# Optimization experiments

Hardware: AMD Instinct MI355X
Metric: run time of the kernel (lower is better)

## Reference

```python
import jax, jax.numpy as jnp
import numpy as np

B, N, F, K, H = 2, 1024, 64, 8, 4
M1 = K + 1                # 9
M2 = (F - 1) * K + 1      # 505
TEMP = 1.0


def setup_inputs() -> dict:
    key = jax.random.key(0)
    ks = jax.random.split(key, 8)
    x = jax.random.normal(ks[0], (B, N, F), dtype=jnp.float32)
    # Bernoulli(0.05) dense adjacency
    adj = (jax.random.uniform(ks[1], (B, N, N)) < 0.05).astype(jnp.float32)
    mask = jnp.ones((B, N), dtype=jnp.float32)
    Wl = jax.random.normal(ks[2], (F, K * H), dtype=jnp.float32) * 0.05
    bl = jnp.zeros((K * H,), dtype=jnp.float32)
    Wr = jax.random.normal(ks[3], (F, K * H), dtype=jnp.float32) * 0.05
    br = jnp.zeros((K * H,), dtype=jnp.float32)
    # fixed affine layer: y = x @ aff_w + aff_b, aff_w[:, :F] = -I, aff_b[M2] = 1
    aff_w = jnp.zeros((F, M1 * M2), dtype=jnp.float32).at[:, :F].set(-jnp.eye(F, dtype=jnp.float32))
    aff_b = jnp.zeros((M1 * M2,), dtype=jnp.float32).at[M2].set(1.0)
    Wm = jax.random.normal(ks[4], (M1 * M2, F), dtype=jnp.float32) * 0.02
    bm = jnp.zeros((F,), dtype=jnp.float32)
    return dict(x=x, adj=adj, mask=mask, Wl=Wl, bl=bl, Wr=Wr, br=br,
                aff_w=aff_w, aff_b=aff_b, Wm=Wm, bm=bm)


def reference(x, adj, mask, Wl, bl, Wr, br, aff_w, aff_b, Wm, bm):
    # --- multi-head edge attention ---
    x_l = (x @ Wl + bl).reshape(B, N, K, H)   # [B,N,K,H]
    x_r = (x @ Wr + br).reshape(B, N, K, H)
    # scores[b,i,j,n,g] = leaky_relu(x_l[b,j] + x_r[b,i]) / temp
    scores = jax.nn.leaky_relu(x_l[:, None, :, :, :] + x_r[:, :, None, :, :]) / TEMP  # [B,N,N,K,H]
    attn_mask = mask[:, None, :] * mask[:, :, None]                # [B,N,N]
    scores = jnp.where(attn_mask[..., None, None] == 0, -1e9, scores)
    att = jax.nn.softmax(scores, axis=2)                           # softmax over source nodes j
    att = jnp.maximum(att * adj[..., None, None], 1e-6)            # clamp(min=1e-6) STE trick
    att = att / jnp.sum(att, axis=2, keepdims=True)                # renormalize
    # --- attention-weighted neighbor gather ---
    x_h = x.reshape(B, N, H, F // H)
    agg = jnp.einsum('bjgk,bijng->bingk', x_h, att).reshape(B, N, K, F)  # [B,N,K,F]
    # --- fixed affine + FFT log-domain geometric mean ---
    x_aff = (agg @ aff_w + aff_b).reshape(B, N, K, M1, M2)
    x_fft = jnp.fft.fft2(x_aff)                                    # over (M1,M2)
    mag = jnp.exp(jnp.mean(jnp.log(jnp.abs(x_fft) + 1e-6), axis=2))  # [B,N,M1,M2]
    ang = jnp.sum(jnp.angle(x_fft), axis=2)
    x_agg = jnp.fft.ifft2(mag * jnp.exp(1j * ang)).real.reshape(B, N, M1 * M2)
    # --- output MLP + node mask ---
    out = x_agg @ Wm + bm
    return out * mask[..., None]
```

## Files before the change

kernel.cpp:

```cpp
#include <hip/hip_runtime.h>
#include <math.h>

#define NN 1024
#define FD 64
#define CH 32
#define M1D 9
#define M2D 505
#define QH 253
#define THALF 2273
#define KPAD 4608
#define KSPLIT 16
#define KCHUNK 288
#define G1SZ 291456
#define G1KS 8

#define FSQRT(x) __builtin_amdgcn_sqrtf(x)
#define FRCP(x)  __builtin_amdgcn_rcpf(x)

typedef short short8 __attribute__((ext_vector_type(8)));
typedef float f32x4 __attribute__((ext_vector_type(4)));

__device__ __forceinline__ unsigned short f2bf(float x) {
    unsigned int u = __builtin_bit_cast(unsigned int, x);
    return (unsigned short)((u + 0x7FFFu + ((u >> 16) & 1u)) >> 16);
}

#define OFF_WP    1024
#define OFF_SUMX  1056
#define OFF_G1    1184
#define OFF_GMT   292640
#define OFF_XL    440096
#define OFF_XR    505632
#define OFF_AGG   571168
#define OFF_PART  1619744
#define OFF_Y     3716896
#define OFF_A2    8435488
#define OFF_WT    16824096
#define OFF_G1P   16856864

__global__ __launch_bounds__(256) void build_tw_kernel(float* __restrict__ T,
                                                       float* __restrict__ Wt,
                                                       float* __restrict__ wp,
                                                       float* __restrict__ sumx) {
    int idx = blockIdx.x * 256 + threadIdx.x;
    if (blockIdx.x == 0) {
        if (threadIdx.x < M1D) {
            float ang = (float)threadIdx.x * (-6.2831853f / 9.0f);
            float s, c; __sincosf(ang, &s, &c);
            wp[2*threadIdx.x] = c; wp[2*threadIdx.x+1] = s;
        }
        if (threadIdx.x >= 64 && threadIdx.x < 192) sumx[threadIdx.x - 64] = 0.f;
    }
    if (idx < 506 * 512) {
        int r = idx >> 9, m2 = idx & 511;
        float v = 0.f;
        if (m2 < M2D) {
            int q = r >> 1;
            int t = (q * m2) % M2D;
            float ang = (float)t * (-6.2831853f / 505.0f);
            float s, c; __sincosf(ang, &s, &c);
            v = (r & 1) ? -s : c;
        }
        T[idx] = v;
    } else if (idx < 506 * 512 + 64 * 512) {
        int i2 = idx - 506 * 512;
        int m = i2 >> 9, col = i2 & 511;
        float v = 0.f;
        if (col < 506) {
            int q = col >> 1;
            int t = (q * m) % M2D;
            float ang = (float)t * (-6.2831853f / 505.0f);
            float s, c; __sincosf(ang, &s, &c);
            v = (col & 1) ? s : c;
        }
        Wt[i2] = v;
    }
}

__global__ __launch_bounds__(64) void proj_kernel(const float* __restrict__ x,
                                                  const float* __restrict__ Wl, const float* __restrict__ bl,
                                                  const float* __restrict__ Wr, const float* __restrict__ br,
                                                  float* __restrict__ xl, float* __restrict__ xr,
                                                  float* __restrict__ sumx) {
    int blk = blockIdx.x, tid = threadIdx.x;
    if (blk >= 2048) {
        int bb = blk - 2048;
        int b = bb >> 4, chunk = bb & 15;
        const float* xb = x + (size_t)b * NN * FD;
        float acc = 0.f;
        int j0 = chunk * 64;
        #pragma unroll 4
        for (int j = j0; j < j0 + 64; j++) acc += xb[j*FD + tid];
        atomicAdd(&sumx[b*FD + tid], acc);
        return;
    }
    int node = blk;
    __shared__ float xrow[FD];
    xrow[tid] = x[(size_t)node*FD + tid];
    __syncthreads();
    int c = tid & 31;
    const float* W = (tid < 32) ? Wl : Wr;
    float acc = (tid < 32) ? bl[c] : br[c];
    #pragma unroll
    for (int f = 0; f < FD; f++) acc += xrow[f] * W[f*CH + c];
    float* dst = (tid < 32) ? xl : xr;
    dst[(size_t)node*CH + c] = acc;
}

__global__ __launch_bounds__(256) void g1_gemm_kernel(const float* __restrict__ T,
                                                      const float* __restrict__ Wm,
                                                      float* __restrict__ G1p) {
    int mt = blockIdx.x, m1 = blockIdx.y, ks = blockIdx.z;
    int tid = threadIdx.x;
    __shared__ float As[64][68];
    __shared__ float Bs[64][64];
    int r0 = mt * 64, k0 = ks * 64;
    const float* Wmb = Wm + (size_t)m1 * M2D * FD;
    float ra[16], rb[16];
    #pragma unroll
    for (int i = 0; i < 16; i++) {
        int l = tid + i*256;
        int r = l >> 6, k = l & 63;
        int rr = r0 + r;
        ra[i] = (rr < 506) ? T[(size_t)rr*512 + k0 + k] : 0.f;
    }
    #pragma unroll
    for (int i = 0; i < 16; i++) {
        int l = tid + i*256;
        int k = l >> 6, f = l & 63;
        int krow = k0 + k;
        rb[i] = (krow < M2D) ? Wmb[(size_t)krow*FD + f] : 0.f;
    }
    #pragma unroll
    for (int i = 0; i < 16; i++) {
        int l = tid + i*256;
        As[l & 63][l >> 6] = ra[i];
    }
    #pragma unroll
    for (int i = 0; i < 16; i++) {
        int l = tid + i*256;
        Bs[l >> 6][l & 63] = rb[i];
    }
    __syncthreads();
    float acc[4][4] = {{0.f}};
    int tm = (tid >> 4) * 4, tf = (tid & 15) * 4;
    #pragma unroll 8
    for (int k = 0; k < 64; k++) {
        float4 a = *(const float4*)&As[k][tm];
        float4 b = *(const float4*)&Bs[k][tf];
        acc[0][0] += a.x*b.x; acc[0][1] += a.x*b.y; acc[0][2] += a.x*b.z; acc[0][3] += a.x*b.w;
        acc[1][0] += a.y*b.x; acc[1][1] += a.y*b.y; acc[1][2] += a.y*b.z; acc[1][3] += a.y*b.w;
        acc[2][0] += a.z*b.x; acc[2][1] += a.z*b.y; acc[2][2] += a.z*b.z; acc[2][3] += a.z*b.w;
        acc[3][0] += a.w*b.x; acc[3][1] += a.w*b.y; acc[3][2] += a.w*b.z; acc[3][3] += a.w*b.w;
    }
    float* G1k = G1p + (size_t)ks * G1SZ;
    #pragma unroll
    for (int i = 0; i < 4; i++) {
        int r = r0 + tm + i;
        if (r >= 506) continue;
        int q = r >> 1, reim = r & 1;
        size_t base = (size_t)(m1*QH + q) * 128;
        #pragma unroll
        for (int j = 0; j < 4; j++)
            G1k[base + (tf + j)*2 + reim] = acc[i][j];
    }
}

__global__ __launch_bounds__(256) void g1_reduce_kernel(const float* __restrict__ G1p,
                                                        float* __restrict__ G1) {
    int idx = blockIdx.x * 256 + threadIdx.x;
    if (idx >= G1SZ/4) return;
    const float4* p = (const float4*)G1p;
    float4 s = p[idx];
    #pragma unroll
    for (int ks = 1; ks < G1KS; ks++) {
        float4 v = p[(size_t)ks*(G1SZ/4) + idx];
        s.x += v.x; s.y += v.y; s.z += v.z; s.w += v.w;
    }
    ((float4*)G1)[idx] = s;
}

__global__ __launch_bounds__(64) void gmat_kernel(const float* __restrict__ G1,
                                                  const float* __restrict__ wp,
                                                  unsigned short* __restrict__ GmT) {
    int t = blockIdx.x;
    int f = threadIdx.x;
    if (t >= THALF) {
        *(unsigned int*)&GmT[(size_t)f*KPAD + 2*t] = 0u;
        return;
    }
    int p, q;
    if (t < QH) { p = 0; q = t; }
    else { int u = t - QH; p = 1 + u / M2D; q = u % M2D; }
    float gr = 0.f, gi = 0.f;
    #pragma unroll
    for (int m1 = 0; m1 < M1D; m1++) {
        float ar, ai;
        if (q < QH) { size_t o = ((size_t)(m1*QH + q)*FD + f)*2; ar = G1[o]; ai = G1[o+1]; }
        else        { size_t o = ((size_t)(m1*QH + (M2D - q))*FD + f)*2; ar = G1[o]; ai = -G1[o+1]; }
        int pm = (p * m1) % M1D;
        float cr = wp[2*pm], ci = -wp[2*pm+1];
        gr += ar*cr - ai*ci;
        gi += ar*ci + ai*cr;
    }
    float scale = (t == 0) ? (1.0f/4545.0f) : (2.0f/4545.0f);
    unsigned int pk = (unsigned int)f2bf(gr*scale) | ((unsigned int)f2bf(-gi*scale) << 16);
    *(unsigned int*)&GmT[(size_t)f*KPAD + 2*t] = pk;
}

__global__ __launch_bounds__(256) void attn_agg_kernel(const float* __restrict__ x,
                                                       const float* __restrict__ adj,
                                                       const float* __restrict__ xl,
                                                       const float* __restrict__ xr,
                                                       const float* __restrict__ sumx,
                                                       float* __restrict__ agg) {
    int node = blockIdx.x;
    int b = node >> 10;
    int tid = threadIdx.x;
    __shared__ float xr_s[CH], Zinv[CH], Sinv[CH];
    __shared__ float red16[16][CH];
    __shared__ int act_list[NN + 8];
    __shared__ int act_n;
    __shared__ float qv2[64][CH];

    if (tid < CH) xr_s[tid] = xr[(size_t)node*CH + tid];
    if (tid == 0) act_n = 0;
    __syncthreads();

    int c = tid & 31, jl = tid >> 5;
    const float* xlb = xl + ((size_t)b << 10) * CH;
    const float* adjrow = adj + (size_t)node * NN;

    int c2 = tid & 15, jl16 = tid >> 4;
    const float2* xlb2 = (const float2*)xlb;
    float xrcx = xr_s[2*c2], xrcy = xr_s[2*c2+1];
    float zx = 0.f, zy = 0.f;
    for (int j0 = jl16; j0 < NN; j0 += 128) {
        float2 sv[8];
        #pragma unroll
        for (int u = 0; u < 8; u++) sv[u] = xlb2[(size_t)(j0 + u*16)*16 + c2];
        #pragma unroll
        for (int u = 0; u < 8; u++) {
            float s0 = sv[u].x + xrcx; s0 = s0 > 0.f ? s0 : 0.01f * s0;
            float s1 = sv[u].y + xrcy; s1 = s1 > 0.f ? s1 : 0.01f * s1;
            zx += __expf(s0); zy += __expf(s1);
        }
    }
    red16[jl16][2*c2]   = zx;
    red16[jl16][2*c2+1] = zy;

    float av[4];
    #pragma unroll
    for (int u = 0; u < 4; u++) av[u] = adjrow[tid + u*256];
    __syncthreads();
    if (tid < CH) {
        float z = 0.f;
        #pragma unroll
        for (int r = 0; r < 16; r++) z += red16[r][tid];
        Zinv[tid] = FRCP(z);
    }
    #pragma unroll
    for (int u = 0; u < 4; u++)
        if (av[u] != 0.f) { int p = atomicAdd(&act_n, 1); act_list[p] = tid + u*256; }
    __syncthreads();
    int nact = act_n;

    int f = tid & 63, n0 = tid >> 6;
    int g = f >> 4;
    int c0 = n0*4 + g, c1 = (n0+4)*4 + g;
    const float* xb = x + ((size_t)b << 10) * FD;
    float acc0 = 0.f, acc1 = 0.f, sacc = 0.f;

    for (int base = 0; base < nact; base += 64) {
        int cnt = min(64, nact - base);
        int cntp = (cnt + 7) & ~7;
        for (int u = tid; u < (cnt << 5); u += 256) {
            int jj = u >> 5, cc = u & 31;
            int j = act_list[base + jj];
            float s = xlb[j*CH + cc] + xr_s[cc];
            s = s > 0.f ? s : 0.01f * s;
            float pv = __expf(s) * Zinv[cc];
            float qq = fmaxf(pv, 1e-6f) - 1e-6f;
            qv2[jj][cc] = qq;
            sacc += qq;
        }
        for (int u = tid + (cnt << 5); u < (cntp << 5); u += 256)
            qv2[u >> 5][u & 31] = 0.f;
        if (tid < cntp - cnt) act_list[base + cnt + tid] = act_list[base];
        __syncthreads();
        for (int jb = 0; jb < cntp; jb += 8) {
            float xv[8];
            #pragma unroll
            for (int u = 0; u < 8; u++) xv[u] = xb[act_list[base + jb + u]*FD + f];
            #pragma unroll
            for (int u = 0; u < 8; u++) {
                acc0 += qv2[jb+u][c0] * xv[u];
                acc1 += qv2[jb+u][c1] * xv[u];
            }
        }
        __syncthreads();
    }
    red16[jl][c] = sacc;
    __syncthreads();
    if (tid < CH) {
        float s = 0.f;
        #pragma unroll
        for (int r = 0; r < 8; r++) s += red16[r][tid];
        Sinv[tid] = FRCP(s + (float)NN * 1e-6f);
    }
    __syncthreads();
    float sx = sumx[b*FD + f] * 1e-6f;
    agg[(size_t)node*512 + n0*FD + f]       = (acc0 + sx) * Sinv[c0];
    agg[(size_t)node*512 + (n0+4)*FD + f]   = (acc1 + sx) * Sinv[c1];
}

__global__ __launch_bounds__(256) void a_gemm_kernel(const float* __restrict__ agg,
                                                     const float* __restrict__ Wt,
                                                     float* __restrict__ A2) {
    int mt = blockIdx.x, nt = blockIdx.y;
    int tid = threadIdx.x;
    __shared__ float As2[64][68];
    __shared__ float Bs[64][64];
    float acc[4][4] = {{0.f}};
    int tm = (tid >> 4) * 4, tf = (tid & 15) * 4;
    float ra[16], rb[16];
    #pragma unroll
    for (int i = 0; i < 16; i++) {
        int l = tid + i*256;
        int r = l >> 6, k = l & 63;
        ra[i] = agg[(size_t)(mt*64 + r)*64 + k];
    }
    #pragma unroll
    for (int i = 0; i < 16; i++) {
        int l = tid + i*256;
        int k = l >> 6, cc = l & 63;
        rb[i] = Wt[(size_t)k*512 + nt*64 + cc];
    }
    #pragma unroll
    for (int i = 0; i < 16; i++) {
        int l = tid + i*256;
        As2[l & 63][l >> 6] = ra[i];
    }
    #pragma unroll
    for (int i = 0; i < 16; i++) {
        int l = tid + i*256;
        Bs[l >> 6][l & 63] = rb[i];
    }
    __syncthreads();
    #pragma unroll 8
    for (int k = 0; k < 64; k++) {
        float4 a = *(const float4*)&As2[k][tm];
        float4 b = *(const float4*)&Bs[k][tf];
        acc[0][0] += a.x*b.x; acc[0][1] += a.x*b.y; acc[0][2] += a.x*b.z; acc[0][3] += a.x*b.w;
        acc[1][0] += a.y*b.x; acc[1][1] += a.y*b.y; acc[1][2] += a.y*b.z; acc[1][3] += a.y*b.w;
        acc[2][0] += a.z*b.x; acc[2][1] += a.z*b.y; acc[2][2] += a.z*b.z; acc[2][3] += a.z*b.w;
        acc[3][0] += a.w*b.x; acc[3][1] += a.w*b.y; acc[3][2] += a.w*b.z; acc[3][3] += a.w*b.w;
    }
    #pragma unroll
    for (int i = 0; i < 4; i++) {
        float4 v = make_float4(acc[i][0], acc[i][1], acc[i][2], acc[i][3]);
        *(float4*)&A2[(size_t)(mt*64 + tm + i)*512 + nt*64 + tf] = v;
    }
}

__global__ __launch_bounds__(256) void y_kernel(const float* __restrict__ A2,
                                                unsigned short* __restrict__ Yb) {
    int node = blockIdx.x;
    int tid = threadIdx.x;
    __shared__ float2 AL[8][QH];

    const float2* A2c = (const float2*)(A2 + (size_t)(node*8)*512);
    float2 rl[8];
    #pragma unroll
    for (int i = 0; i < 8; i++) {
        int idx = tid + i*256;
        rl[i] = (idx < 8*QH) ? A2c[(idx/QH)*256 + (idx%QH)] : make_float2(0.f, 0.f);
    }
    #pragma unroll
    for (int i = 0; i < 8; i++) {
        int idx = tid + i*256;
        if (idx < 8*QH) AL[idx/QH][idx%QH] = rl[i];
    }
    __syncthreads();

    unsigned short* Yrow = Yb + (size_t)node * KPAD;
    if (tid < (KPAD - 2*THALF)/2) *(unsigned int*)&Yrow[2*THALF + 2*tid] = 0u;

    const float CPt[5] = {1.0f, 0.766044443119f, 0.173648177667f, -0.5f, -0.939692620786f};
    const float SPt[5] = {0.0f, -0.642787609687f, -0.984807753012f, -0.866025403784f, -0.342020143326f};

    #define Y_BODY(P, Q, QQ, CSIGN)                                            \
    {                                                                          \
        float cp = CPt[P], sp = SPt[P];                                        \
        float Pr = 1.f, Pi = 0.f, rp2 = 1.f;                                   \
        _Pragma("unroll")                                                      \
        for (int n = 0; n < 8; n++) {                                          \
            float2 Av = AL[n][QQ];                                             \
            float Ar = Av.x, Ai = (CSIGN) * Av.y;                              \
            float Xr = cp - Ar, Xi = sp - Ai;                                  \
            rp2 *= (Xr*Xr + Xi*Xi);                                            \
            float nPr = Pr*Xr - Pi*Xi;                                         \
            Pi = Pr*Xi + Pi*Xr; Pr = nPr;                                      \
        }                                                                      \
        float pAbs = FSQRT(Pr*Pr + Pi*Pi);                                     \
        float rp8 = FSQRT(FSQRT(FSQRT(FSQRT(rp2))));                           \
        float s = rp8 * FRCP(fmaxf(pAbs, 1e-20f));                             \
        int t = (P == 0) ? (Q) : (QH + ((P)-1)*M2D + (Q));                     \
        unsigned int pk = (unsigned int)f2bf(s*Pr) | ((unsigned int)f2bf(s*Pi) << 16); \
        *(unsigned int*)&Yrow[2*t] = pk;                                       \
    }

    if (tid < QH) Y_BODY(0, tid, tid, 1.f);
    #pragma unroll
    for (int p = 1; p <= 4; p++) {
        {
            int q = tid;
            int qq = (q < QH) ? q : (M2D - q);
            float cs = (q < QH) ? 1.f : -1.f;
            Y_BODY(p, q, qq, cs);
        }
        {
            int q = tid + 256;
            if (q < M2D) {
                int qq = M2D - q;
                Y_BODY(p, q, qq, -1.f);
            }
        }
    }
    #undef Y_BODY
}

__global__ __launch_bounds__(256) void gemm_kernel(const unsigned short* __restrict__ Yb,
                                                   const unsigned short* __restrict__ GmT,
                                                   float* __restrict__ part) {
    int mtile = blockIdx.x, kc = blockIdx.y;
    int tid = threadIdx.x;
    __shared__ unsigned short Ys[64*40];
    __shared__ unsigned short Gs[64*40];
    int m0 = mtile * 64;
    int k0 = kc * KCHUNK;
    int r = tid >> 2, kg = (tid & 3) * 8;
    const unsigned short* Ysrc = Yb + (size_t)(m0 + r)*KPAD + k0 + kg;
    const unsigned short* Gsrc = GmT + (size_t)r*KPAD + k0 + kg;
    uint4 ya = *(const uint4*)Ysrc;
    uint4 ga = *(const uint4*)Gsrc;
    int w = tid >> 6, lane = tid & 63;
    int lm = lane & 15, quad = lane >> 4;
    f32x4 acc0 = {0.f,0.f,0.f,0.f}, acc1 = acc0, acc2 = acc0, acc3 = acc0;
    for (int ks = 0; ks < KCHUNK; ks += 32) {
        *(uint4*)&Ys[r*40 + kg] = ya;
        *(uint4*)&Gs[r*40 + kg] = ga;
        __syncthreads();
        if (ks + 32 < KCHUNK) {
            ya = *(const uint4*)(Ysrc + ks + 32);
            ga = *(const uint4*)(Gsrc + ks + 32);
        }
        short8 b  = *(const short8*)&Gs[(w*16 + lm)*40 + quad*8];
        short8 a0 = *(const short8*)&Ys[(lm)*40      + quad*8];
        short8 a1 = *(const short8*)&Ys[(16 + lm)*40 + quad*8];
        short8 a2 = *(const short8*)&Ys[(32 + lm)*40 + quad*8];
        short8 a3 = *(const short8*)&Ys[(48 + lm)*40 + quad*8];
        acc0 = __builtin_amdgcn_mfma_f32_16x16x32_bf16(a0, b, acc0, 0, 0, 0);
        acc1 = __builtin_amdgcn_mfma_f32_16x16x32_bf16(a1, b, acc1, 0, 0, 0);
        acc2 = __builtin_amdgcn_mfma_f32_16x16x32_bf16(a2, b, acc2, 0, 0, 0);
        acc3 = __builtin_amdgcn_mfma_f32_16x16x32_bf16(a3, b, acc3, 0, 0, 0);
        __syncthreads();
    }
    float* prow = part + (size_t)kc * (2048*FD);
    int col = w*16 + lm;
    #pragma unroll
    for (int rr = 0; rr < 4; rr++) {
        int row = quad*4 + rr;
        prow[(size_t)(m0 + row)*FD + col]      = acc0[rr];
        prow[(size_t)(m0 + 16 + row)*FD + col] = acc1[rr];
        prow[(size_t)(m0 + 32 + row)*FD + col] = acc2[rr];
        prow[(size_t)(m0 + 48 + row)*FD + col] = acc3[rr];
    }
}

__global__ __launch_bounds__(256) void reduce_kernel(const float* __restrict__ part,
                                                     const float* __restrict__ bm,
                                                     const float* __restrict__ mask,
                                                     float* __restrict__ out) {
    int idx = blockIdx.x * 256 + threadIdx.x;
    if (idx >= 32768) return;
    const float4* p4 = (const float4*)part;
    float4 s = p4[idx];
    #pragma unroll
    for (int kc = 1; kc < KSPLIT; kc++) {
        float4 v = p4[(size_t)kc*32768 + idx];
        s.x += v.x; s.y += v.y; s.z += v.z; s.w += v.w;
    }
    int f0 = (idx & 15) * 4;
    int node = idx >> 4;
    float mk = mask[node];
    s.x = (s.x + bm[f0])   * mk;
    s.y = (s.y + bm[f0+1]) * mk;
    s.z = (s.z + bm[f0+2]) * mk;
    s.w = (s.w + bm[f0+3]) * mk;
    ((float4*)out)[idx] = s;
}

extern "C" void kernel_launch(void* const* d_in, const int* in_sizes, int n_in,
                              void* d_out, int out_size, void* d_ws, size_t ws_size,
                              hipStream_t stream) {
    const float* x    = (const float*)d_in[0];
    const float* adj  = (const float*)d_in[1];
    const float* mask = (const float*)d_in[2];
    const float* Wl   = (const float*)d_in[3];
    const float* bl   = (const float*)d_in[4];
    const float* Wr   = (const float*)d_in[5];
    const float* br   = (const float*)d_in[6];
    const float* Wm   = (const float*)d_in[9];
    const float* bm   = (const float*)d_in[10];
    float* out = (float*)d_out;
    float* ws  = (float*)d_ws;

    float* wp   = ws + OFF_WP;
    float* sumx = ws + OFF_SUMX;
    float* G1   = ws + OFF_G1;
    unsigned short* GmT = (unsigned short*)(ws + OFF_GMT);
    float* xl   = ws + OFF_XL;
    float* xr   = ws + OFF_XR;
    float* agg  = ws + OFF_AGG;
    float* part = ws + OFF_PART;
    float* T    = ws + OFF_Y;
    unsigned short* Yb = (unsigned short*)(ws + OFF_Y);
    float* A2   = ws + OFF_A2;
    float* Wt   = ws + OFF_WT;
    float* G1p  = ws + OFF_G1P;

    hipLaunchKernelGGL(build_tw_kernel, dim3((506*512 + 64*512 + 255)/256), dim3(256), 0, stream, T, Wt, wp, sumx);
    hipLaunchKernelGGL(proj_kernel, dim3(2080), dim3(64), 0, stream, x, Wl, bl, Wr, br, xl, xr, sumx);
    hipLaunchKernelGGL(g1_gemm_kernel, dim3(8, 9, G1KS), dim3(256), 0, stream, T, Wm, G1p);
    hipLaunchKernelGGL(g1_reduce_kernel, dim3((G1SZ/4 + 255)/256), dim3(256), 0, stream, G1p, G1);
    hipLaunchKernelGGL(gmat_kernel, dim3(KPAD/2), dim3(64), 0, stream, G1, wp, GmT);
    hipLaunchKernelGGL(attn_agg_kernel, dim3(2048), dim3(256), 0, stream, x, adj, xl, xr, sumx, agg);
    hipLaunchKernelGGL(a_gemm_kernel, dim3(256, 8), dim3(256), 0, stream, agg, Wt, A2);
    hipLaunchKernelGGL(y_kernel, dim3(2048), dim3(256), 0, stream, A2, Yb);
    hipLaunchKernelGGL(gemm_kernel, dim3(32, KSPLIT), dim3(256), 0, stream, Yb, GmT, part);
    hipLaunchKernelGGL(reduce_kernel, dim3(128), dim3(256), 0, stream, part, bm, mask, out);
}
```

Baseline: 188.9 us.

## Fuse A-GEMM with Y product kernel and fold G1 split-K reduce into gmat

Folds the split-K reduction of G1 partials directly into gmat_kernel, which removes the g1_reduce launch and the G1 buffer. Merges a_gemm and y_kernel so each block computes a 64x64 tile of A2, stages it in shared memory, and immediately builds the bf16 Y rows for its 8 nodes and 32 frequency bins, including mirrored bins. This avoids writing and re-reading the large fp32 A2 intermediate and saves a launch. The cost is redundant G1p reads in gmat (8 partials times 9 per output) and a different thread mapping for the Y computation.

New measurement: 177.8 us, median of 2. 5.9% less time.

```diff
diff --git a/kernel.cpp b/kernel.cpp
--- a/kernel.cpp
+++ b/kernel.cpp
@@ -27,16 +27,14 @@
 
 #define OFF_WP    1024
 #define OFF_SUMX  1056
-#define OFF_G1    1184
-#define OFF_GMT   292640
-#define OFF_XL    440096
-#define OFF_XR    505632
-#define OFF_AGG   571168
-#define OFF_PART  1619744
-#define OFF_Y     3716896
-#define OFF_A2    8435488
-#define OFF_WT    16824096
-#define OFF_G1P   16856864
+#define OFF_GMT   1184
+#define OFF_XL    148640
+#define OFF_XR    214176
+#define OFF_AGG   279712
+#define OFF_PART  1328288
+#define OFF_Y     3425440
+#define OFF_WT    8144032
+#define OFF_G1P   8176800
 
 __global__ __launch_bounds__(256) void build_tw_kernel(float* __restrict__ T,
                                                        float* __restrict__ Wt,
@@ -166,21 +164,7 @@
     }
 }
 
-__global__ __launch_bounds__(256) void g1_reduce_kernel(const float* __restrict__ G1p,
-                                                        float* __restrict__ G1) {
-    int idx = blockIdx.x * 256 + threadIdx.x;
-    if (idx >= G1SZ/4) return;
-    const float4* p = (const float4*)G1p;
-    float4 s = p[idx];
-    #pragma unroll
-    for (int ks = 1; ks < G1KS; ks++) {
-        float4 v = p[(size_t)ks*(G1SZ/4) + idx];
-        s.x += v.x; s.y += v.y; s.z += v.z; s.w += v.w;
-    }
-    ((float4*)G1)[idx] = s;
-}
-
-__global__ __launch_bounds__(64) void gmat_kernel(const float* __restrict__ G1,
+__global__ __launch_bounds__(64) void gmat_kernel(const float* __restrict__ G1p,
                                                   const float* __restrict__ wp,
                                                   unsigned short* __restrict__ GmT) {
     int t = blockIdx.x;
@@ -192,12 +176,19 @@
     int p, q;
     if (t < QH) { p = 0; q = t; }
     else { int u = t - QH; p = 1 + u / M2D; q = u % M2D; }
+    int qq = (q < QH) ? q : (M2D - q);
+    float sgn = (q < QH) ? 1.f : -1.f;
     float gr = 0.f, gi = 0.f;
     #pragma unroll
     for (int m1 = 0; m1 < M1D; m1++) {
-        float ar, ai;
-        if (q < QH) { size_t o = ((size_t)(m1*QH + q)*FD + f)*2; ar = G1[o]; ai = G1[o+1]; }
-        else        { size_t o = ((size_t)(m1*QH + (M2D - q))*FD + f)*2; ar = G1[o]; ai = -G1[o+1]; }
+        size_t o = ((size_t)(m1*QH + qq)*FD + f)*2;
+        float ar = 0.f, ai = 0.f;
+        #pragma unroll
+        for (int ks = 0; ks < G1KS; ks++) {
+            ar += G1p[(size_t)ks*G1SZ + o];
+            ai += G1p[(size_t)ks*G1SZ + o + 1];
+        }
+        ai *= sgn;
         int pm = (p * m1) % M1D;
         float cr = wp[2*pm], ci = -wp[2*pm+1];
         gr += ar*cr - ai*ci;
@@ -314,21 +305,20 @@
     agg[(size_t)node*512 + (n0+4)*FD + f]   = (acc1 + sx) * Sinv[c1];
 }
 
-__global__ __launch_bounds__(256) void a_gemm_kernel(const float* __restrict__ agg,
-                                                     const float* __restrict__ Wt,
-                                                     float* __restrict__ A2) {
-    int mt = blockIdx.x, nt = blockIdx.y;
+__global__ __launch_bounds__(256) void ay_kernel(const float* __restrict__ agg,
+                                                 const float* __restrict__ Wt,
+                                                 unsigned short* __restrict__ Yb) {
+    int slab = blockIdx.x, nt = blockIdx.y;
     int tid = threadIdx.x;
     __shared__ float As2[64][68];
     __shared__ float Bs[64][64];
-    float acc[4][4] = {{0.f}};
     int tm = (tid >> 4) * 4, tf = (tid & 15) * 4;
     float ra[16], rb[16];
     #pragma unroll
     for (int i = 0; i < 16; i++) {
         int l = tid + i*256;
         int r = l >> 6, k = l & 63;
-        ra[i] = agg[(size_t)(mt*64 + r)*64 + k];
+        ra[i] = agg[(size_t)(slab*64 + r)*64 + k];
     }
     #pragma unroll
     for (int i = 0; i < 16; i++) {
@@ -337,16 +327,11 @@
         rb[i] = Wt[(size_t)k*512 + nt*64 + cc];
     }
     #pragma unroll
-    for (int i = 0; i < 16; i++) {
-        int l = tid + i*256;
-        As2[l & 63][l >> 6] = ra[i];
-    }
-    #pragma unroll
-    for (int i = 0; i < 16; i++) {
-        int l = tid + i*256;
-        Bs[l >> 6][l & 63] = rb[i];
-    }
-    __syncthreads();
+    for (int i = 0; i < 16; i++) { int l = tid + i*256; As2[l & 63][l >> 6] = ra[i]; }
+    #pragma unroll
+    for (int i = 0; i < 16; i++) { int l = tid + i*256; Bs[l >> 6][l & 63] = rb[i]; }
+    __syncthreads();
+    float acc[4][4] = {{0.f}};
     #pragma unroll 8
     for (int k = 0; k < 64; k++) {
         float4 a = *(const float4*)&As2[k][tm];
@@ -356,78 +341,61 @@
         acc[2][0] += a.z*b.x; acc[2][1] += a.z*b.y; acc[2][2] += a.z*b.z; acc[2][3] += a.z*b.w;
         acc[3][0] += a.w*b.x; acc[3][1] += a.w*b.y; acc[3][2] += a.w*b.z; acc[3][3] += a.w*b.w;
     }
-    #pragma unroll
-    for (int i = 0; i < 4; i++) {
-        float4 v = make_float4(acc[i][0], acc[i][1], acc[i][2], acc[i][3]);
-        *(float4*)&A2[(size_t)(mt*64 + tm + i)*512 + nt*64 + tf] = v;
-    }
-}
-
-__global__ __launch_bounds__(256) void y_kernel(const float* __restrict__ A2,
-                                                unsigned short* __restrict__ Yb) {
-    int node = blockIdx.x;
-    int tid = threadIdx.x;
-    __shared__ float2 AL[8][QH];
-
-    const float2* A2c = (const float2*)(A2 + (size_t)(node*8)*512);
-    float2 rl[8];
-    #pragma unroll
-    for (int i = 0; i < 8; i++) {
-        int idx = tid + i*256;
-        rl[i] = (idx < 8*QH) ? A2c[(idx/QH)*256 + (idx%QH)] : make_float2(0.f, 0.f);
-    }
-    #pragma unroll
-    for (int i = 0; i < 8; i++) {
-        int idx = tid + i*256;
-        if (idx < 8*QH) AL[idx/QH][idx%QH] = rl[i];
-    }
-    __syncthreads();
-
-    unsigned short* Yrow = Yb + (size_t)node * KPAD;
-    if (tid < (KPAD - 2*THALF)/2) *(unsigned int*)&Yrow[2*THALF + 2*tid] = 0u;
-
-    const float CPt[5] = {1.0f, 0.766044443119f, 0.173648177667f, -0.5f, -0.939692620786f};
-    const float SPt[5] = {0.0f, -0.642787609687f, -0.984807753012f, -0.866025403784f, -0.342020143326f};
-
-    #define Y_BODY(P, Q, QQ, CSIGN)                                            \
-    {                                                                          \
-        float cp = CPt[P], sp = SPt[P];                                        \
-        float Pr = 1.f, Pi = 0.f, rp2 = 1.f;                                   \
-        _Pragma("unroll")                                                      \
-        for (int n = 0; n < 8; n++) {                                          \
-            float2 Av = AL[n][QQ];                                             \
-            float Ar = Av.x, Ai = (CSIGN) * Av.y;                              \
-            float Xr = cp - Ar, Xi = sp - Ai;                                  \
-            rp2 *= (Xr*Xr + Xi*Xi);                                            \
-            float nPr = Pr*Xr - Pi*Xi;                                         \
-            Pi = Pr*Xi + Pi*Xr; Pr = nPr;                                      \
-        }                                                                      \
-        float pAbs = FSQRT(Pr*Pr + Pi*Pi);                                     \
-        float rp8 = FSQRT(FSQRT(FSQRT(FSQRT(rp2))));                           \
-        float s = rp8 * FRCP(fmaxf(pAbs, 1e-20f));                             \
-        int t = (P == 0) ? (Q) : (QH + ((P)-1)*M2D + (Q));                     \
-        unsigned int pk = (unsigned int)f2bf(s*Pr) | ((unsigned int)f2bf(s*Pi) << 16); \
-        *(unsigned int*)&Yrow[2*t] = pk;                                       \
-    }
-
-    if (tid < QH) Y_BODY(0, tid, tid, 1.f);
-    #pragma unroll
-    for (int p = 1; p <= 4; p++) {
-        {
-            int q = tid;
-            int qq = (q < QH) ? q : (M2D - q);
-            float cs = (q < QH) ? 1.f : -1.f;
-            Y_BODY(p, q, qq, cs);
-        }
-        {
-            int q = tid + 256;
-            if (q < M2D) {
-                int qq = M2D - q;
-                Y_BODY(p, q, qq, -1.f);
+    __syncthreads();
+    #pragma unroll
+    for (int i = 0; i < 4; i++)
+        #pragma unroll
+        for (int j = 0; j < 4; j++)
+            As2[tm + i][tf + j] = acc[i][j];
+    __syncthreads();
+
+    int qloc = tid & 31, node = tid >> 5;
+    unsigned short* Yrow = Yb + (size_t)(slab*8 + node)*KPAD;
+    int q = nt*32 + qloc;
+
+    if (q <= 252) {
+        float2 Av[8];
+        #pragma unroll
+        for (int n = 0; n < 8; n++)
+            Av[n] = make_float2(As2[node*8 + n][2*qloc], As2[node*8 + n][2*qloc + 1]);
+
+        const float CPt[5] = {1.0f, 0.766044443119f, 0.173648177667f, -0.5f, -0.939692620786f};
+        const float SPt[5] = {0.0f, -0.642787609687f, -0.984807753012f, -0.866025403784f, -0.342020143326f};
+
+        #define Y_PROD(CSIGN, TIDX)                                            \
+        {                                                                      \
+            float Pr = 1.f, Pi = 0.f, rp2 = 1.f;                               \
+            _Pragma("unroll")                                                  \
+            for (int n = 0; n < 8; n++) {                                      \
+                float Xr = cp - Av[n].x, Xi = sp - (CSIGN) * Av[n].y;          \
+                rp2 *= (Xr*Xr + Xi*Xi);                                        \
+                float nPr = Pr*Xr - Pi*Xi;                                     \
+                Pi = Pr*Xi + Pi*Xr; Pr = nPr;                                  \
+            }                                                                  \
+            float pAbs = FSQRT(Pr*Pr + Pi*Pi);                                 \
+            float rp8 = FSQRT(FSQRT(FSQRT(FSQRT(rp2))));                       \
+            float s = rp8 * FRCP(fmaxf(pAbs, 1e-20f));                         \
+            unsigned int pk = (unsigned int)f2bf(s*Pr) | ((unsigned int)f2bf(s*Pi) << 16); \
+            *(unsigned int*)&Yrow[2*(TIDX)] = pk;                              \
+        }
+
+        #pragma unroll
+        for (int p = 0; p < 5; p++) {
+            float cp = CPt[p], sp = SPt[p];
+            int tfwd = (p == 0) ? q : (QH + (p-1)*M2D + q);
+            Y_PROD(1.f, tfwd);
+            if (p >= 1 && q >= 1) {
+                int tmir = QH + (p-1)*M2D + (M2D - q);
+                Y_PROD(-1.f, tmir);
             }
         }
-    }
-    #undef Y_BODY
+        #undef Y_PROD
+    }
+    if (nt == 7 && tid < 248) {
+        int rr = tid / 31, cc2 = tid % 31;
+        unsigned short* Yr2 = Yb + (size_t)(slab*8 + rr)*KPAD;
+        *(unsigned int*)&Yr2[2*THALF + 2*cc2] = 0u;
+    }
 }
 
 __global__ __launch_bounds__(256) void gemm_kernel(const unsigned short* __restrict__ Yb,
@@ -518,7 +486,6 @@
 
     float* wp   = ws + OFF_WP;
     float* sumx = ws + OFF_SUMX;
-    float* G1   = ws + OFF_G1;
     unsigned short* GmT = (unsigned short*)(ws + OFF_GMT);
     float* xl   = ws + OFF_XL;
     float* xr   = ws + OFF_XR;
@@ -526,18 +493,15 @@
     float* part = ws + OFF_PART;
     float* T    = ws + OFF_Y;
     unsigned short* Yb = (unsigned short*)(ws + OFF_Y);
-    float* A2   = ws + OFF_A2;
     float* Wt   = ws + OFF_WT;
     float* G1p  = ws + OFF_G1P;
 
     hipLaunchKernelGGL(build_tw_kernel, dim3((506*512 + 64*512 + 255)/256), dim3(256), 0, stream, T, Wt, wp, sumx);
     hipLaunchKernelGGL(proj_kernel, dim3(2080), dim3(64), 0, stream, x, Wl, bl, Wr, br, xl, xr, sumx);
     hipLaunchKernelGGL(g1_gemm_kernel, dim3(8, 9, G1KS), dim3(256), 0, stream, T, Wm, G1p);
-    hipLaunchKernelGGL(g1_reduce_kernel, dim3((G1SZ/4 + 255)/256), dim3(256), 0, stream, G1p, G1);
-    hipLaunchKernelGGL(gmat_kernel, dim3(KPAD/2), dim3(64), 0, stream, G1, wp, GmT);
+    hipLaunchKernelGGL(gmat_kernel, dim3(KPAD/2), dim3(64), 0, stream, G1p, wp, GmT);
     hipLaunchKernelGGL(attn_agg_kernel, dim3(2048), dim3(256), 0, stream, x, adj, xl, xr, sumx, agg);
-    hipLaunchKernelGGL(a_gemm_kernel, dim3(256, 8), dim3(256), 0, stream, agg, Wt, A2);
-    hipLaunchKernelGGL(y_kernel, dim3(2048), dim3(256), 0, stream, A2, Yb);
+    hipLaunchKernelGGL(ay_kernel, dim3(256, 8), dim3(256), 0, stream, agg, Wt, Yb);
     hipLaunchKernelGGL(gemm_kernel, dim3(32, KSPLIT), dim3(256), 0, stream, Yb, GmT, part);
     hipLaunchKernelGGL(reduce_kernel, dim3(128), dim3(256), 0, stream, part, bm, mask, out);
 }
```
